# Performance work log

Measured on AMD Instinct MI355X. Metric: run time of the kernel, lower is better.

The kernel has to match this reference:

```python
import jax, jax.numpy as jnp
import numpy as np

# Fixed architecture constants (from source / MambaConfig)
B_ = 8          # batch
L_ = 2048       # seq_len
D_MODEL = 6     # input_size / d_model
ED = 48         # expand_factor * d_model = hidden_size
N = 32          # d_state
DCONV = 16      # d_conv
NLAYERS = 4
DTRANK = 1      # ceil(d_model/16)
NCLASSES = 4
EPS = 1e-5


def setup_inputs() -> dict:
    key = jax.random.key(0)
    ks = jax.random.split(key, 10)
    def rn(k, shape, s=0.1):
        return jax.random.normal(k, shape, jnp.float32) * s
    return {
        "x": jax.random.normal(ks[0], (B_, L_, D_MODEL), jnp.float32),
        "in_proj_w": rn(ks[1], (NLAYERS, 2 * ED, D_MODEL)),
        "conv_w": rn(ks[2], (NLAYERS, ED, DCONV)),
        "conv_b": jnp.zeros((NLAYERS, ED), jnp.float32),
        "x_proj_w": rn(ks[3], (NLAYERS, DTRANK + 2 * N, ED)),
        "dt_proj_w": rn(ks[4], (NLAYERS, ED, DTRANK)),
        "dt_proj_b": rn(ks[5], (NLAYERS, ED), 0.05),
        "A_log": jnp.tile(jnp.log(jnp.arange(1, N + 1, dtype=jnp.float32)), (NLAYERS, ED, 1)),
        "D": jnp.ones((NLAYERS, ED), jnp.float32),
        "out_proj_w": rn(ks[6], (NLAYERS, D_MODEL, ED)),
        "norm_w": jnp.ones((NLAYERS, D_MODEL), jnp.float32),
        "fc_w": rn(ks[7], (NCLASSES, ED)),
        "fc_b": jnp.zeros((NCLASSES,), jnp.float32),
    }


def _dw_conv(x, w, b):
    # x: [B, L, ED], depthwise causal conv over L with kernel DCONV
    x_n = x.transpose(0, 2, 1)            # [B, ED, L]
    k = w[:, None, :]                      # [ED, 1, DCONV]
    y = jax.lax.conv_general_dilated(
        x_n, k, window_strides=(1,), padding=[(DCONV - 1, 0)],
        feature_group_count=ED, dimension_numbers=("NCH", "OIH", "NCH"))
    return (y + b[None, :, None]).transpose(0, 2, 1)  # [B, L, ED]


def _ssm(x_c, delta, A, Bm, Cm, Dp):
    # selective scan: h_t = exp(delta_t A) h_{t-1} + delta_t B_t x_t ; y_t = C_t . h_t + D x_t
    deltaA = jnp.exp(delta[..., None] * A)                    # [B,L,ED,N]
    deltaBx = (delta * x_c)[..., None] * Bm[:, :, None, :]    # [B,L,ED,N]
    def comb(c1, c2):
        a1, b1 = c1
        a2, b2 = c2
        return (a1 * a2, a2 * b1 + b2)
    _, h = jax.lax.associative_scan(comb, (deltaA, deltaBx), axis=1)
    y = jnp.einsum("blen,bln->ble", h, Cm) + Dp * x_c
    return y


def reference(x, in_proj_w, conv_w, conv_b, x_proj_w, dt_proj_w, dt_proj_b,
              A_log, D, out_proj_w, norm_w, fc_w, fc_b):
    h = x
    inner = None
    for i in range(NLAYERS):
        # RMSNorm (pre-norm)
        xn = h * jax.lax.rsqrt(jnp.mean(h * h, axis=-1, keepdims=True) + EPS) * norm_w[i]
        xz = xn @ in_proj_w[i].T                               # [B,L,2*ED]
        x_in, z = jnp.split(xz, 2, axis=-1)
        x_c = jax.nn.silu(_dw_conv(x_in, conv_w[i], conv_b[i]))
        dbl = x_c @ x_proj_w[i].T                              # [B,L,DTRANK+2N]
        dr = dbl[..., :DTRANK]
        Bm = dbl[..., DTRANK:DTRANK + N]
        Cm = dbl[..., DTRANK + N:]
        delta = jax.nn.softplus(dr @ dt_proj_w[i].T + dt_proj_b[i])  # [B,L,ED]
        A = -jnp.exp(A_log[i])                                 # [ED,N]
        y = _ssm(x_c, delta, A, Bm, Cm, D[i])
        y = y * jax.nn.silu(z)                                 # [B,L,ED]
        if i == NLAYERS - 1:
            inner = y  # classifier mode: keep 48-dim inner hidden
        else:
            h = y @ out_proj_w[i].T + h                        # residual in d_model
    last_hidden = inner[:, -1, :]                              # [B,ED]
    return last_hidden @ fc_w.T + fc_b                         # [B,NCLASSES]
```

## Files before the change

kernel.cpp:

```cpp
#include <hip/hip_runtime.h>
#include <math.h>

#define B_ 8
#define L_ 2048
#define DM 6
#define ED 48
#define NS 32
#define DCONV 16
#define NLAYERS 4
#define NCLASSES 4
#define EPS 1e-5f

#define CH 32
#define CL (L_ / CH)


__global__ void __launch_bounds__(256) k_fused_pre(
    const float* __restrict__ x,
    const float* __restrict__ yprev,
    const float* __restrict__ outw,
    const float* __restrict__ hin,
    float* __restrict__ hout,
    const float* __restrict__ ipw,
    const float* __restrict__ nw,
    const float* __restrict__ cw,
    const float* __restrict__ cb,
    const float* __restrict__ xpw,
    const float* __restrict__ dtw,
    const float* __restrict__ dtb,
    float* __restrict__ z,
    float* __restrict__ xcg,
    float* __restrict__ delta,
    float* __restrict__ Bm, float* __restrict__ Cm,
    int layer)
{
    __shared__ float sh[DM][48];
    __shared__ float sxin[ED][48];
    __shared__ float sxc[ED][33];
    __shared__ float srn[48];
    __shared__ float sdr[32];

    int b  = blockIdx.x >> 6;
    int l0 = (blockIdx.x & 63) * 32;
    int tid = threadIdx.x;

    for (int i = tid; i < DM * 47; i += 256) {
        int d = i / 47;
        int p = i % 47;
        int l = l0 - 15 + p;
        float hv = 0.f;
        if (l >= 0) {
            if (layer == 0) {
                hv = x[((size_t)b * L_ + l) * DM + d];
            } else {
                hv = hin[((size_t)b * DM + d) * L_ + l];
                const float* yp = yprev + (size_t)b * ED * L_ + l;
                const float* wp = outw + d * ED;
                float acc = 0.f;
#pragma unroll
                for (int e = 0; e < ED; ++e) acc += yp[(size_t)e * L_] * wp[e];
                hv += acc;
            }
            if (p >= 15 && layer < NLAYERS - 1)
                hout[((size_t)b * DM + d) * L_ + l] = hv;
        }
        sh[d][p] = hv;
    }
    __syncthreads();

    if (tid < 47) {
        float ss = 0.f;
#pragma unroll
        for (int d = 0; d < DM; ++d) ss += sh[d][tid] * sh[d][tid];
        srn[tid] = rsqrtf(ss * (1.f / DM) + EPS);
    }
    __syncthreads();

    for (int i = tid; i < ED * 47; i += 256) {
        int e = i / 47, p = i % 47;
        const float* wp = ipw + e * DM;
        float acc = 0.f;
#pragma unroll
        for (int d = 0; d < DM; ++d) acc += sh[d][p] * nw[d] * wp[d];
        sxin[e][p] = acc * srn[p];
    }
    for (int i = tid; i < ED * 32; i += 256) {
        int e = i >> 5, po = i & 31;
        int p = po + 15;
        const float* wp = ipw + (ED + e) * DM;
        float acc = 0.f;
#pragma unroll
        for (int d = 0; d < DM; ++d) acc += sh[d][p] * nw[d] * wp[d];
        z[((size_t)b * ED + e) * L_ + l0 + po] = acc * srn[p];
    }
    __syncthreads();

    for (int i = tid; i < ED * 32; i += 256) {
        int e = i >> 5, po = i & 31;
        const float* wp = cw + e * DCONV;
        float acc = cb[e];
#pragma unroll
        for (int k = 0; k < DCONV; ++k) acc += sxin[e][po + k] * wp[k];
        float v = acc / (1.f + __expf(-acc));
        sxc[e][po] = v;
        xcg[((size_t)b * ED + e) * L_ + l0 + po] = v;
    }
    __syncthreads();

    {
        int og = tid >> 5, li = tid & 31;
        int isB = og < 4;
        int nb = isB ? og * 8 : (og - 4) * 8;
        int rowBase = isB ? (1 + nb) : (1 + NS + nb);
        const float* wr = xpw + rowBase * ED;
        float a0=0,a1=0,a2=0,a3=0,a4=0,a5=0,a6=0,a7=0, dr=0;
#pragma unroll 4
        for (int e = 0; e < ED; ++e) {
            float xv = sxc[e][li];
            a0 += xv * wr[0*ED+e]; a1 += xv * wr[1*ED+e];
            a2 += xv * wr[2*ED+e]; a3 += xv * wr[3*ED+e];
            a4 += xv * wr[4*ED+e]; a5 += xv * wr[5*ED+e];
            a6 += xv * wr[6*ED+e]; a7 += xv * wr[7*ED+e];
            dr += xv * xpw[e];
        }
        float* outp = (isB ? Bm : Cm) + ((size_t)(b * L_ + l0 + li)) * NS + nb;
        ((float4*)outp)[0] = make_float4(a0, a1, a2, a3);
        ((float4*)outp)[1] = make_float4(a4, a5, a6, a7);
        if (og == 0) sdr[li] = dr;
    }
    __syncthreads();

    for (int i = tid; i < ED * 32; i += 256) {
        int e = i >> 5, po = i & 31;
        float s = sdr[po] * dtw[e] + dtb[e];
        delta[((size_t)b * ED + e) * L_ + l0 + po] =
            fmaxf(s, 0.f) + log1pf(__expf(-fabsf(s)));
    }
}

__global__ void __launch_bounds__(256) k_scan1(
    const float* __restrict__ delta, const float* __restrict__ xc,
    const float* __restrict__ Bm,
    const float* __restrict__ A_log,
    float* __restrict__ sumA, float* __restrict__ sumH)
{
    int t = blockIdx.x * blockDim.x + threadIdx.x;
    int n = t & 31;
    int g = t >> 5;
    if (g >= B_ * ED * CH) return;
    int chunk = g % CH;
    int be    = g / CH;
    int e = be % ED;
    int b = be / ED;
    float A = -__expf(A_log[e * NS + n]);
    size_t eRow = (size_t)(b * ED + e) * L_ + chunk * CL;
    const float4* dRow = (const float4*)(delta + eRow);
    const float4* xRow = (const float4*)(xc + eRow);
    const float* bBase = Bm + ((size_t)b * L_ + chunk * CL) * NS + n;
    float h = 0.f, sd = 0.f;
#pragma unroll 4
    for (int q = 0; q < CL / 4; ++q) {
        float4 d4 = dRow[q];
        float4 x4 = xRow[q];
        float b0 = bBase[(4 * q + 0) * NS];
        float b1 = bBase[(4 * q + 1) * NS];
        float b2 = bBase[(4 * q + 2) * NS];
        float b3 = bBase[(4 * q + 3) * NS];
        h = __expf(d4.x * A) * h + (d4.x * x4.x) * b0;
        h = __expf(d4.y * A) * h + (d4.y * x4.y) * b1;
        h = __expf(d4.z * A) * h + (d4.z * x4.z) * b2;
        h = __expf(d4.w * A) * h + (d4.w * x4.w) * b3;
        sd += d4.x + d4.y + d4.z + d4.w;
    }
    sumA[g * NS + n] = __expf(A * sd);
    sumH[g * NS + n] = h;
}

__global__ void __launch_bounds__(256) k_scan3(
    const float* __restrict__ delta, const float* __restrict__ xc,
    const float* __restrict__ Bm, const float* __restrict__ Cm,
    const float* __restrict__ z,
    const float* __restrict__ A_log,
    const float* __restrict__ Dp,
    const float* __restrict__ sumA, const float* __restrict__ sumH,
    float* __restrict__ y)
{
    int t = blockIdx.x * blockDim.x + threadIdx.x;
    int n = t & 31;
    int g = t >> 5;
    if (g >= B_ * ED * CH) return;
    int chunk = g % CH;
    int be    = g / CH;
    int e = be % ED;
    int b = be / ED;
    float A  = -__expf(A_log[e * NS + n]);
    float Dv = Dp[e];

    float h = 0.f;
    int base = be * CH;
    for (int c = 0; c < chunk; ++c) {
        int idx = (base + c) * NS + n;
        h = sumA[idx] * h + sumH[idx];
    }

    size_t eRow = (size_t)(b * ED + e) * L_ + chunk * CL;
    size_t nRow = ((size_t)b * L_ + chunk * CL) * NS + n;
    const float4* dRow = (const float4*)(delta + eRow);
    const float4* xRow = (const float4*)(xc + eRow);
    const float* bBase = Bm + nRow;
    const float* cBase = Cm + nRow;
    const float* zRow  = z + eRow;
    float*       yRow  = y + eRow;
    int s0 = n & 1, s1 = n & 2;
    for (int q = 0; q < CL / 4; ++q) {
        float4 d4 = dRow[q];
        float4 x4 = xRow[q];
        float bb0 = bBase[(4 * q + 0) * NS];
        float bb1 = bBase[(4 * q + 1) * NS];
        float bb2 = bBase[(4 * q + 2) * NS];
        float bb3 = bBase[(4 * q + 3) * NS];
        float cc0 = cBase[(4 * q + 0) * NS];
        float cc1 = cBase[(4 * q + 1) * NS];
        float cc2 = cBase[(4 * q + 2) * NS];
        float cc3 = cBase[(4 * q + 3) * NS];
        h = __expf(d4.x * A) * h + (d4.x * x4.x) * bb0;  float p0 = h * cc0;
        h = __expf(d4.y * A) * h + (d4.y * x4.y) * bb1;  float p1 = h * cc1;
        h = __expf(d4.z * A) * h + (d4.z * x4.z) * bb2;  float p2 = h * cc2;
        h = __expf(d4.w * A) * h + (d4.w * x4.w) * bb3;  float p3 = h * cc3;
        float u  = s0 ? p1 : p0;
        float us = s0 ? p0 : p1;
        u += __shfl_xor(us, 1, 32);
        float v  = s0 ? p3 : p2;
        float vs = s0 ? p2 : p3;
        v += __shfl_xor(vs, 1, 32);
        float wv  = s1 ? v : u;
        float wvs = s1 ? u : v;
        wv += __shfl_xor(wvs, 2, 32);
        wv += __shfl_xor(wv, 4, 32);
        wv += __shfl_xor(wv, 8, 32);
        wv += __shfl_xor(wv, 16, 32);
        if (n < 4) {
            int l4 = q * 4;
            float xs = (n == 0) ? x4.x : (n == 1) ? x4.y : (n == 2) ? x4.z : x4.w;
            float yr = wv + Dv * xs;
            float zv = zRow[l4 + n];
            yRow[l4 + n] = yr * (zv / (1.f + __expf(-zv)));
        }
    }
}

__global__ void k_cls(const float* __restrict__ y,
                      const float* __restrict__ fcw,
                      const float* __restrict__ fcb,
                      float* __restrict__ out)
{
    int t = threadIdx.x;
    if (t >= B_ * NCLASSES) return;
    int b = t / NCLASSES;
    int c = t - b * NCLASSES;
    const float* yp = y + (size_t)b * ED * L_ + (L_ - 1);
    const float* wp = fcw + c * ED;
    float acc = fcb[c];
#pragma unroll
    for (int e = 0; e < ED; ++e) acc += yp[(size_t)e * L_] * wp[e];
    out[t] = acc;
}

extern "C" void kernel_launch(void* const* d_in, const int* in_sizes, int n_in,
                              void* d_out, int out_size, void* d_ws, size_t ws_size,
                              hipStream_t stream)
{
    const float* x          = (const float*)d_in[0];
    const float* in_proj_w  = (const float*)d_in[1];
    const float* conv_w     = (const float*)d_in[2];
    const float* conv_b     = (const float*)d_in[3];
    const float* x_proj_w   = (const float*)d_in[4];
    const float* dt_proj_w  = (const float*)d_in[5];
    const float* dt_proj_b  = (const float*)d_in[6];
    const float* A_log      = (const float*)d_in[7];
    const float* Dp         = (const float*)d_in[8];
    const float* out_proj_w = (const float*)d_in[9];
    const float* norm_w     = (const float*)d_in[10];
    const float* fc_w       = (const float*)d_in[11];
    const float* fc_b       = (const float*)d_in[12];

    float* ws   = (float*)d_ws;
    float* z    = ws;
    float* xc   = z    + B_ * ED * L_;
    float* delta= xc   + B_ * ED * L_;
    float* y    = delta+ B_ * ED * L_;
    float* Bmat = y    + B_ * ED * L_;
    float* Cmat = Bmat + B_ * L_ * NS;
    float* hA   = Cmat + B_ * L_ * NS;
    float* hB   = hA   + B_ * DM * L_;
    float* sumA = hB   + B_ * DM * L_;
    float* sumH = sumA + B_ * ED * CH * NS;

    const int nScanT = B_ * ED * CH * NS;

    for (int i = 0; i < NLAYERS; ++i) {
        float* hout      = (i & 1) ? hB : hA;
        const float* hin = (i == 0) ? nullptr : ((i & 1) ? hA : hB);
        const float* ow  = (i == 0) ? out_proj_w : out_proj_w + (size_t)(i - 1) * DM * ED;
        k_fused_pre<<<B_ * (L_ / 32), 256, 0, stream>>>(
            x, y, ow, hin, hout,
            in_proj_w + (size_t)i * 96 * DM, norm_w + (size_t)i * DM,
            conv_w + (size_t)i * ED * DCONV, conv_b + (size_t)i * ED,
            x_proj_w + (size_t)i * 65 * ED,
            dt_proj_w + (size_t)i * ED, dt_proj_b + (size_t)i * ED,
            z, xc, delta, Bmat, Cmat, i);
        k_scan1<<<(nScanT + 255) / 256, 256, 0, stream>>>(
            delta, xc, Bmat, A_log + (size_t)i * ED * NS, sumA, sumH);
        k_scan3<<<(nScanT + 255) / 256, 256, 0, stream>>>(
            delta, xc, Bmat, Cmat, z,
            A_log + (size_t)i * ED * NS, Dp + (size_t)i * ED, sumA, sumH, y);
    }
    k_cls<<<1, 64, 0, stream>>>(y, fc_w, fc_b, (float*)d_out);
}
```

Before: 343.3 us.

## Fuse all layers into one persistent kernel with hierarchical grid barriers

```diff
diff --git a/kernel.cpp b/kernel.cpp
--- a/kernel.cpp
+++ b/kernel.cpp
@@ -13,257 +13,307 @@
 
 #define CH 32
 #define CL (L_ / CH)
-
-
-__global__ void __launch_bounds__(256) k_fused_pre(
+#define NBLK 512
+#define NSCANTASK ((B_ * ED * CH * NS) / 256)
+
+#define WS_FLOATS 5177344
+#define BAR_EPOCHS 12
+#define BAR_SLOT_U32 16
+#define BAR_SLOTS 9
+#define BAR_BYTES (BAR_EPOCHS * BAR_SLOTS * BAR_SLOT_U32 * 4)
+
+__device__ __forceinline__ void grid_barrier(unsigned* bar, int epoch)
+{
+    __syncthreads();
+    if (threadIdx.x == 0) {
+        unsigned* leaf   = bar + (epoch * BAR_SLOTS + (blockIdx.x & 7)) * BAR_SLOT_U32;
+        unsigned* master = bar + (epoch * BAR_SLOTS + 8) * BAR_SLOT_U32;
+        __threadfence();
+        if (atomicAdd(leaf, 1u) == (NBLK / 8) - 1)
+            atomicAdd(master, 1u);
+        while (__hip_atomic_load(master, __ATOMIC_ACQUIRE,
+                                 __HIP_MEMORY_SCOPE_AGENT) < 8u)
+            __builtin_amdgcn_s_sleep(8);
+        __threadfence();
+    }
+    __syncthreads();
+}
+
+__global__ void __launch_bounds__(256, 2) k_all(
     const float* __restrict__ x,
-    const float* __restrict__ yprev,
-    const float* __restrict__ outw,
-    const float* __restrict__ hin,
-    float* __restrict__ hout,
-    const float* __restrict__ ipw,
-    const float* __restrict__ nw,
-    const float* __restrict__ cw,
-    const float* __restrict__ cb,
-    const float* __restrict__ xpw,
-    const float* __restrict__ dtw,
-    const float* __restrict__ dtb,
-    float* __restrict__ z,
-    float* __restrict__ xcg,
-    float* __restrict__ delta,
-    float* __restrict__ Bm, float* __restrict__ Cm,
-    int layer)
+    const float* __restrict__ in_proj_w,
+    const float* __restrict__ conv_w,
+    const float* __restrict__ conv_b,
+    const float* __restrict__ x_proj_w,
+    const float* __restrict__ dt_proj_w,
+    const float* __restrict__ dt_proj_b,
+    const float* __restrict__ A_log,
+    const float* __restrict__ Dp,
+    const float* __restrict__ out_proj_w,
+    const float* __restrict__ norm_w,
+    const float* __restrict__ fc_w,
+    const float* __restrict__ fc_b,
+    float* __restrict__ out,
+    float* __restrict__ ws)
 {
+    float* z     = ws;
+    float* xcg   = z     + (size_t)B_ * ED * L_;
+    float* delta = xcg   + (size_t)B_ * ED * L_;
+    float* y     = delta + (size_t)B_ * ED * L_;
+    float* Bm    = y     + (size_t)B_ * ED * L_;
+    float* Cm    = Bm    + (size_t)B_ * L_ * NS;
+    float* hA    = Cm    + (size_t)B_ * L_ * NS;
+    float* hB    = hA    + (size_t)B_ * DM * L_;
+    float* sumA  = hB    + (size_t)B_ * DM * L_;
+    float* sumH  = sumA  + (size_t)B_ * ED * CH * NS;
+    unsigned* bar = (unsigned*)(ws + WS_FLOATS);
+
     __shared__ float sh[DM][48];
     __shared__ float sxin[ED][48];
     __shared__ float sxc[ED][33];
     __shared__ float srn[48];
     __shared__ float sdr[32];
 
-    int b  = blockIdx.x >> 6;
-    int l0 = (blockIdx.x & 63) * 32;
-    int tid = threadIdx.x;
-
-    for (int i = tid; i < DM * 47; i += 256) {
-        int d = i / 47;
-        int p = i % 47;
-        int l = l0 - 15 + p;
-        float hv = 0.f;
-        if (l >= 0) {
-            if (layer == 0) {
-                hv = x[((size_t)b * L_ + l) * DM + d];
+    const int tid = threadIdx.x;
+
+    for (int layer = 0; layer < NLAYERS; ++layer) {
+        const float* ipw = in_proj_w + (size_t)layer * 96 * DM;
+        const float* nw  = norm_w    + (size_t)layer * DM;
+        const float* cw  = conv_w    + (size_t)layer * ED * DCONV;
+        const float* cb  = conv_b    + (size_t)layer * ED;
+        const float* xpw = x_proj_w  + (size_t)layer * 65 * ED;
+        const float* dtw = dt_proj_w + (size_t)layer * ED;
+        const float* dtb = dt_proj_b + (size_t)layer * ED;
+        const float* al  = A_log     + (size_t)layer * ED * NS;
+        const float* dpp = Dp        + (size_t)layer * ED;
+        const float* ow  = (layer == 0) ? out_proj_w
+                          : out_proj_w + (size_t)(layer - 1) * DM * ED;
+        float* hout      = (layer & 1) ? hB : hA;
+        const float* hin = (layer & 1) ? hA : hB;
+
+        {
+            const int b  = blockIdx.x >> 6;
+            const int l0 = (blockIdx.x & 63) * 32;
+
+            if (layer > 0) {
+                for (int i = tid; i < ED * 47; i += 256) {
+                    int e = i / 47, p = i % 47;
+                    int l = l0 - 15 + p;
+                    sxin[e][p] = (l >= 0)
+                        ? y[((size_t)b * ED + e) * L_ + l] : 0.f;
+                }
+                __syncthreads();
+                for (int i = tid; i < DM * 47; i += 256) {
+                    int d = i / 47, p = i % 47;
+                    int l = l0 - 15 + p;
+                    float hv = 0.f;
+                    if (l >= 0) {
+                        hv = hin[((size_t)b * DM + d) * L_ + l];
+                        const float* wp = ow + d * ED;
+                        float acc = 0.f;
+#pragma unroll
+                        for (int e = 0; e < ED; ++e) acc += sxin[e][p] * wp[e];
+                        hv += acc;
+                        if (p >= 15 && layer < NLAYERS - 1)
+                            hout[((size_t)b * DM + d) * L_ + l] = hv;
+                    }
+                    sh[d][p] = hv;
+                }
             } else {
-                hv = hin[((size_t)b * DM + d) * L_ + l];
-                const float* yp = yprev + (size_t)b * ED * L_ + l;
-                const float* wp = outw + d * ED;
+                for (int i = tid; i < DM * 47; i += 256) {
+                    int d = i / 47, p = i % 47;
+                    int l = l0 - 15 + p;
+                    float hv = 0.f;
+                    if (l >= 0) {
+                        hv = x[((size_t)b * L_ + l) * DM + d];
+                        if (p >= 15)
+                            hout[((size_t)b * DM + d) * L_ + l] = hv;
+                    }
+                    sh[d][p] = hv;
+                }
+            }
+            __syncthreads();
+
+            if (tid < 47) {
+                float ss = 0.f;
+#pragma unroll
+                for (int d = 0; d < DM; ++d) ss += sh[d][tid] * sh[d][tid];
+                srn[tid] = rsqrtf(ss * (1.f / DM) + EPS);
+            }
+            __syncthreads();
+
+            for (int i = tid; i < ED * 47; i += 256) {
+                int e = i / 47, p = i % 47;
+                const float* wp = ipw + e * DM;
                 float acc = 0.f;
 #pragma unroll
-                for (int e = 0; e < ED; ++e) acc += yp[(size_t)e * L_] * wp[e];
-                hv += acc;
-            }
-            if (p >= 15 && layer < NLAYERS - 1)
-                hout[((size_t)b * DM + d) * L_ + l] = hv;
+                for (int d = 0; d < DM; ++d) acc += sh[d][p] * nw[d] * wp[d];
+                sxin[e][p] = acc * srn[p];
+            }
+            for (int i = tid; i < ED * 32; i += 256) {
+                int e = i >> 5, po = i & 31;
+                int p = po + 15;
+                const float* wp = ipw + (ED + e) * DM;
+                float acc = 0.f;
+#pragma unroll
+                for (int d = 0; d < DM; ++d) acc += sh[d][p] * nw[d] * wp[d];
+                z[((size_t)b * ED + e) * L_ + l0 + po] = acc * srn[p];
+            }
+            __syncthreads();
+
+            for (int i = tid; i < ED * 32; i += 256) {
+                int e = i >> 5, po = i & 31;
+                const float* wp = cw + e * DCONV;
+                float acc = cb[e];
+#pragma unroll
+                for (int k = 0; k < DCONV; ++k) acc += sxin[e][po + k] * wp[k];
+                float v = acc / (1.f + __expf(-acc));
+                sxc[e][po] = v;
+                xcg[((size_t)b * ED + e) * L_ + l0 + po] = v;
+            }
+            __syncthreads();
+
+            {
+                int og = tid >> 5, li = tid & 31;
+                int isB = og < 4;
+                int nb = isB ? og * 8 : (og - 4) * 8;
+                int rowBase = isB ? (1 + nb) : (1 + NS + nb);
+                const float* wr = xpw + rowBase * ED;
+                float a0=0,a1=0,a2=0,a3=0,a4=0,a5=0,a6=0,a7=0, dr=0;
+#pragma unroll 4
+                for (int e = 0; e < ED; ++e) {
+                    float xv = sxc[e][li];
+                    a0 += xv * wr[0*ED+e]; a1 += xv * wr[1*ED+e];
+                    a2 += xv * wr[2*ED+e]; a3 += xv * wr[3*ED+e];
+                    a4 += xv * wr[4*ED+e]; a5 += xv * wr[5*ED+e];
+                    a6 += xv * wr[6*ED+e]; a7 += xv * wr[7*ED+e];
+                    dr += xv * xpw[e];
+                }
+                float* outp = (isB ? Bm : Cm) + ((size_t)(b * L_ + l0 + li)) * NS + nb;
+                ((float4*)outp)[0] = make_float4(a0, a1, a2, a3);
+                ((float4*)outp)[1] = make_float4(a4, a5, a6, a7);
+                if (og == 0) sdr[li] = dr;
+            }
+            __syncthreads();
+
+            for (int i = tid; i < ED * 32; i += 256) {
+                int e = i >> 5, po = i & 31;
+                float s = sdr[po] * dtw[e] + dtb[e];
+                delta[((size_t)b * ED + e) * L_ + l0 + po] =
+                    fmaxf(s, 0.f) + log1pf(__expf(-fabsf(s)));
+            }
         }
-        sh[d][p] = hv;
+        grid_barrier(bar, layer * 3 + 0);
+
+        for (int task = blockIdx.x; task < NSCANTASK; task += NBLK) {
+            int t = task * 256 + tid;
+            int n = t & 31;
+            int g = t >> 5;
+            int chunk = g & (CH - 1);
+            int be    = g >> 5;
+            int e = be % ED;
+            int b = be / ED;
+            float A = -__expf(al[e * NS + n]);
+            size_t eRow = (size_t)(b * ED + e) * L_ + chunk * CL;
+            const float4* dRow = (const float4*)(delta + eRow);
+            const float4* xRow = (const float4*)(xcg + eRow);
+            const float* bBase = Bm + ((size_t)b * L_ + chunk * CL) * NS + n;
+            float h = 0.f, sd = 0.f;
+#pragma unroll 4
+            for (int q = 0; q < CL / 4; ++q) {
+                float4 d4 = dRow[q];
+                float4 x4 = xRow[q];
+                float b0 = bBase[(4 * q + 0) * NS];
+                float b1 = bBase[(4 * q + 1) * NS];
+                float b2 = bBase[(4 * q + 2) * NS];
+                float b3 = bBase[(4 * q + 3) * NS];
+                h = __expf(d4.x * A) * h + (d4.x * x4.x) * b0;
+                h = __expf(d4.y * A) * h + (d4.y * x4.y) * b1;
+                h = __expf(d4.z * A) * h + (d4.z * x4.z) * b2;
+                h = __expf(d4.w * A) * h + (d4.w * x4.w) * b3;
+                sd += d4.x + d4.y + d4.z + d4.w;
+            }
+            sumA[g * NS + n] = __expf(A * sd);
+            sumH[g * NS + n] = h;
+        }
+        grid_barrier(bar, layer * 3 + 1);
+
+        for (int task = blockIdx.x; task < NSCANTASK; task += NBLK) {
+            int t = task * 256 + tid;
+            int n = t & 31;
+            int g = t >> 5;
+            int chunk = g & (CH - 1);
+            int be    = g >> 5;
+            int e = be % ED;
+            int b = be / ED;
+            float A  = -__expf(al[e * NS + n]);
+            float Dv = dpp[e];
+
+            float h = 0.f;
+            int base = be * CH;
+            for (int c = 0; c < chunk; ++c) {
+                int idx = (base + c) * NS + n;
+                h = sumA[idx] * h + sumH[idx];
+            }
+
+            size_t eRow = (size_t)(b * ED + e) * L_ + chunk * CL;
+            size_t nRow = ((size_t)b * L_ + chunk * CL) * NS + n;
+            const float4* dRow = (const float4*)(delta + eRow);
+            const float4* xRow = (const float4*)(xcg + eRow);
+            const float* bBase = Bm + nRow;
+            const float* cBase = Cm + nRow;
+            const float* zRow  = z + eRow;
+            float*       yRow  = y + eRow;
+            int s0 = n & 1, s1 = n & 2;
+            for (int q = 0; q < CL / 4; ++q) {
+                float4 d4 = dRow[q];
+                float4 x4 = xRow[q];
+                float bb0 = bBase[(4 * q + 0) * NS];
+                float bb1 = bBase[(4 * q + 1) * NS];
+                float bb2 = bBase[(4 * q + 2) * NS];
+                float bb3 = bBase[(4 * q + 3) * NS];
+                float cc0 = cBase[(4 * q + 0) * NS];
+                float cc1 = cBase[(4 * q + 1) * NS];
+                float cc2 = cBase[(4 * q + 2) * NS];
+                float cc3 = cBase[(4 * q + 3) * NS];
+                h = __expf(d4.x * A) * h + (d4.x * x4.x) * bb0;  float p0 = h * cc0;
+                h = __expf(d4.y * A) * h + (d4.y * x4.y) * bb1;  float p1 = h * cc1;
+                h = __expf(d4.z * A) * h + (d4.z * x4.z) * bb2;  float p2 = h * cc2;
+                h = __expf(d4.w * A) * h + (d4.w * x4.w) * bb3;  float p3 = h * cc3;
+                float u  = s0 ? p1 : p0;
+                float us = s0 ? p0 : p1;
+                u += __shfl_xor(us, 1, 32);
+                float v  = s0 ? p3 : p2;
+                float vs = s0 ? p2 : p3;
+                v += __shfl_xor(vs, 1, 32);
+                float wv  = s1 ? v : u;
+                float wvs = s1 ? u : v;
+                wv += __shfl_xor(wvs, 2, 32);
+                wv += __shfl_xor(wv, 4, 32);
+                wv += __shfl_xor(wv, 8, 32);
+                wv += __shfl_xor(wv, 16, 32);
+                if (n < 4) {
+                    int l4 = q * 4;
+                    float xs = (n == 0) ? x4.x : (n == 1) ? x4.y : (n == 2) ? x4.z : x4.w;
+                    float yr = wv + Dv * xs;
+                    float zv = zRow[l4 + n];
+                    yRow[l4 + n] = yr * (zv / (1.f + __expf(-zv)));
+                }
+            }
+        }
+        grid_barrier(bar, layer * 3 + 2);
     }
-    __syncthreads();
-
-    if (tid < 47) {
-        float ss = 0.f;
-#pragma unroll
-        for (int d = 0; d < DM; ++d) ss += sh[d][tid] * sh[d][tid];
-        srn[tid] = rsqrtf(ss * (1.f / DM) + EPS);
+
+    if (blockIdx.x == 0 && tid < B_ * NCLASSES) {
+        int b = tid / NCLASSES;
+        int c = tid - b * NCLASSES;
+        const float* yp = y + (size_t)b * ED * L_ + (L_ - 1);
+        const float* wp = fc_w + c * ED;
+        float acc = fc_b[c];
+#pragma unroll
+        for (int e = 0; e < ED; ++e) acc += yp[(size_t)e * L_] * wp[e];
+        out[tid] = acc;
     }
-    __syncthreads();
-
-    for (int i = tid; i < ED * 47; i += 256) {
-        int e = i / 47, p = i % 47;
-        const float* wp = ipw + e * DM;
-        float acc = 0.f;
-#pragma unroll
-        for (int d = 0; d < DM; ++d) acc += sh[d][p] * nw[d] * wp[d];
-        sxin[e][p] = acc * srn[p];
-    }
-    for (int i = tid; i < ED * 32; i += 256) {
-        int e = i >> 5, po = i & 31;
-        int p = po + 15;
-        const float* wp = ipw + (ED + e) * DM;
-        float acc = 0.f;
-#pragma unroll
-        for (int d = 0; d < DM; ++d) acc += sh[d][p] * nw[d] * wp[d];
-        z[((size_t)b * ED + e) * L_ + l0 + po] = acc * srn[p];
-    }
-    __syncthreads();
-
-    for (int i = tid; i < ED * 32; i += 256) {
-        int e = i >> 5, po = i & 31;
-        const float* wp = cw + e * DCONV;
-        float acc = cb[e];
-#pragma unroll
-        for (int k = 0; k < DCONV; ++k) acc += sxin[e][po + k] * wp[k];
-        float v = acc / (1.f + __expf(-acc));
-        sxc[e][po] = v;
-        xcg[((size_t)b * ED + e) * L_ + l0 + po] = v;
-    }
-    __syncthreads();
-
-    {
-        int og = tid >> 5, li = tid & 31;
-        int isB = og < 4;
-        int nb = isB ? og * 8 : (og - 4) * 8;
-        int rowBase = isB ? (1 + nb) : (1 + NS + nb);
-        const float* wr = xpw + rowBase * ED;
-        float a0=0,a1=0,a2=0,a3=0,a4=0,a5=0,a6=0,a7=0, dr=0;
-#pragma unroll 4
-        for (int e = 0; e < ED; ++e) {
-            float xv = sxc[e][li];
-            a0 += xv * wr[0*ED+e]; a1 += xv * wr[1*ED+e];
-            a2 += xv * wr[2*ED+e]; a3 += xv * wr[3*ED+e];
-            a4 += xv * wr[4*ED+e]; a5 += xv * wr[5*ED+e];
-            a6 += xv * wr[6*ED+e]; a7 += xv * wr[7*ED+e];
-            dr += xv * xpw[e];
-        }
-        float* outp = (isB ? Bm : Cm) + ((size_t)(b * L_ + l0 + li)) * NS + nb;
-        ((float4*)outp)[0] = make_float4(a0, a1, a2, a3);
-        ((float4*)outp)[1] = make_float4(a4, a5, a6, a7);
-        if (og == 0) sdr[li] = dr;
-    }
-    __syncthreads();
-
-    for (int i = tid; i < ED * 32; i += 256) {
-        int e = i >> 5, po = i & 31;
-        float s = sdr[po] * dtw[e] + dtb[e];
-        delta[((size_t)b * ED + e) * L_ + l0 + po] =
-            fmaxf(s, 0.f) + log1pf(__expf(-fabsf(s)));
-    }
-}
-
-__global__ void __launch_bounds__(256) k_scan1(
-    const float* __restrict__ delta, const float* __restrict__ xc,
-    const float* __restrict__ Bm,
-    const float* __restrict__ A_log,
-    float* __restrict__ sumA, float* __restrict__ sumH)
-{
-    int t = blockIdx.x * blockDim.x + threadIdx.x;
-    int n = t & 31;
-    int g = t >> 5;
-    if (g >= B_ * ED * CH) return;
-    int chunk = g % CH;
-    int be    = g / CH;
-    int e = be % ED;
-    int b = be / ED;
-    float A = -__expf(A_log[e * NS + n]);
-    size_t eRow = (size_t)(b * ED + e) * L_ + chunk * CL;
-    const float4* dRow = (const float4*)(delta + eRow);
-    const float4* xRow = (const float4*)(xc + eRow);
-    const float* bBase = Bm + ((size_t)b * L_ + chunk * CL) * NS + n;
-    float h = 0.f, sd = 0.f;
-#pragma unroll 4
-    for (int q = 0; q < CL / 4; ++q) {
-        float4 d4 = dRow[q];
-        float4 x4 = xRow[q];
-        float b0 = bBase[(4 * q + 0) * NS];
-        float b1 = bBase[(4 * q + 1) * NS];
-        float b2 = bBase[(4 * q + 2) * NS];
-        float b3 = bBase[(4 * q + 3) * NS];
-        h = __expf(d4.x * A) * h + (d4.x * x4.x) * b0;
-        h = __expf(d4.y * A) * h + (d4.y * x4.y) * b1;
-        h = __expf(d4.z * A) * h + (d4.z * x4.z) * b2;
-        h = __expf(d4.w * A) * h + (d4.w * x4.w) * b3;
-        sd += d4.x + d4.y + d4.z + d4.w;
-    }
-    sumA[g * NS + n] = __expf(A * sd);
-    sumH[g * NS + n] = h;
-}
-
-__global__ void __launch_bounds__(256) k_scan3(
-    const float* __restrict__ delta, const float* __restrict__ xc,
-    const float* __restrict__ Bm, const float* __restrict__ Cm,
-    const float* __restrict__ z,
-    const float* __restrict__ A_log,
-    const float* __restrict__ Dp,
-    const float* __restrict__ sumA, const float* __restrict__ sumH,
-    float* __restrict__ y)
-{
-    int t = blockIdx.x * blockDim.x + threadIdx.x;
-    int n = t & 31;
-    int g = t >> 5;
-    if (g >= B_ * ED * CH) return;
-    int chunk = g % CH;
-    int be    = g / CH;
-    int e = be % ED;
-    int b = be / ED;
-    float A  = -__expf(A_log[e * NS + n]);
-    float Dv = Dp[e];
-
-    float h = 0.f;
-    int base = be * CH;
-    for (int c = 0; c < chunk; ++c) {
-        int idx = (base + c) * NS + n;
-        h = sumA[idx] * h + sumH[idx];
-    }
-
-    size_t eRow = (size_t)(b * ED + e) * L_ + chunk * CL;
-    size_t nRow = ((size_t)b * L_ + chunk * CL) * NS + n;
-    const float4* dRow = (const float4*)(delta + eRow);
-    const float4* xRow = (const float4*)(xc + eRow);
-    const float* bBase = Bm + nRow;
-    const float* cBase = Cm + nRow;
-    const float* zRow  = z + eRow;
-    float*       yRow  = y + eRow;
-    int s0 = n & 1, s1 = n & 2;
-    for (int q = 0; q < CL / 4; ++q) {
-        float4 d4 = dRow[q];
-        float4 x4 = xRow[q];
-        float bb0 = bBase[(4 * q + 0) * NS];
-        float bb1 = bBase[(4 * q + 1) * NS];
-        float bb2 = bBase[(4 * q + 2) * NS];
-        float bb3 = bBase[(4 * q + 3) * NS];
-        float cc0 = cBase[(4 * q + 0) * NS];
-        float cc1 = cBase[(4 * q + 1) * NS];
-        float cc2 = cBase[(4 * q + 2) * NS];
-        float cc3 = cBase[(4 * q + 3) * NS];
-        h = __expf(d4.x * A) * h + (d4.x * x4.x) * bb0;  float p0 = h * cc0;
-        h = __expf(d4.y * A) * h + (d4.y * x4.y) * bb1;  float p1 = h * cc1;
-        h = __expf(d4.z * A) * h + (d4.z * x4.z) * bb2;  float p2 = h * cc2;
-        h = __expf(d4.w * A) * h + (d4.w * x4.w) * bb3;  float p3 = h * cc3;
-        float u  = s0 ? p1 : p0;
-        float us = s0 ? p0 : p1;
-        u += __shfl_xor(us, 1, 32);
-        float v  = s0 ? p3 : p2;
-        float vs = s0 ? p2 : p3;
-        v += __shfl_xor(vs, 1, 32);
-        float wv  = s1 ? v : u;
-        float wvs = s1 ? u : v;
-        wv += __shfl_xor(wvs, 2, 32);
-        wv += __shfl_xor(wv, 4, 32);
-        wv += __shfl_xor(wv, 8, 32);
-        wv += __shfl_xor(wv, 16, 32);
-        if (n < 4) {
-            int l4 = q * 4;
-            float xs = (n == 0) ? x4.x : (n == 1) ? x4.y : (n == 2) ? x4.z : x4.w;
-            float yr = wv + Dv * xs;
-            float zv = zRow[l4 + n];
-            yRow[l4 + n] = yr * (zv / (1.f + __expf(-zv)));
-        }
-    }
-}
-
-__global__ void k_cls(const float* __restrict__ y,
-                      const float* __restrict__ fcw,
-                      const float* __restrict__ fcb,
-                      float* __restrict__ out)
-{
-    int t = threadIdx.x;
-    if (t >= B_ * NCLASSES) return;
-    int b = t / NCLASSES;
-    int c = t - b * NCLASSES;
-    const float* yp = y + (size_t)b * ED * L_ + (L_ - 1);
-    const float* wp = fcw + c * ED;
-    float acc = fcb[c];
-#pragma unroll
-    for (int e = 0; e < ED; ++e) acc += yp[(size_t)e * L_] * wp[e];
-    out[t] = acc;
 }
 
 extern "C" void kernel_launch(void* const* d_in, const int* in_sizes, int n_in,
@@ -283,37 +333,11 @@
     const float* norm_w     = (const float*)d_in[10];
     const float* fc_w       = (const float*)d_in[11];
     const float* fc_b       = (const float*)d_in[12];
-
-    float* ws   = (float*)d_ws;
-    float* z    = ws;
-    float* xc   = z    + B_ * ED * L_;
-    float* delta= xc   + B_ * ED * L_;
-    float* y    = delta+ B_ * ED * L_;
-    float* Bmat = y    + B_ * ED * L_;
-    float* Cmat = Bmat + B_ * L_ * NS;
-    float* hA   = Cmat + B_ * L_ * NS;
-    float* hB   = hA   + B_ * DM * L_;
-    float* sumA = hB   + B_ * DM * L_;
-    float* sumH = sumA + B_ * ED * CH * NS;
-
-    const int nScanT = B_ * ED * CH * NS;
-
-    for (int i = 0; i < NLAYERS; ++i) {
-        float* hout      = (i & 1) ? hB : hA;
-        const float* hin = (i == 0) ? nullptr : ((i & 1) ? hA : hB);
-        const float* ow  = (i == 0) ? out_proj_w : out_proj_w + (size_t)(i - 1) * DM * ED;
-        k_fused_pre<<<B_ * (L_ / 32), 256, 0, stream>>>(
-            x, y, ow, hin, hout,
-            in_proj_w + (size_t)i * 96 * DM, norm_w + (size_t)i * DM,
-            conv_w + (size_t)i * ED * DCONV, conv_b + (size_t)i * ED,
-            x_proj_w + (size_t)i * 65 * ED,
-            dt_proj_w + (size_t)i * ED, dt_proj_b + (size_t)i * ED,
-            z, xc, delta, Bmat, Cmat, i);
-        k_scan1<<<(nScanT + 255) / 256, 256, 0, stream>>>(
-            delta, xc, Bmat, A_log + (size_t)i * ED * NS, sumA, sumH);
-        k_scan3<<<(nScanT + 255) / 256, 256, 0, stream>>>(
-            delta, xc, Bmat, Cmat, z,
-            A_log + (size_t)i * ED * NS, Dp + (size_t)i * ED, sumA, sumH, y);
-    }
-    k_cls<<<1, 64, 0, stream>>>(y, fc_w, fc_b, (float*)d_out);
+    float* ws = (float*)d_ws;
+
+    hipMemsetAsync((void*)(ws + WS_FLOATS), 0, BAR_BYTES, stream);
+
+    k_all<<<dim3(NBLK), dim3(256), 0, stream>>>(
+        x, in_proj_w, conv_w, conv_b, x_proj_w, dt_proj_w, dt_proj_b,
+        A_log, Dp, out_proj_w, norm_w, fc_w, fc_b, (float*)d_out, ws);
 }
```

Measured after the change: 997.7 us. 191% more time.
